# Kernel tuning notes

Hardware: AMD Instinct MI355X
Metric: run time of the kernel (lower is better)

The kernel has to match this reference:

```python
import jax, jax.numpy as jnp
import numpy as np
from jax import lax

B, FMAP, ENC, DEC, ATTN = 64, 512, 256, 512, 256
NUM_CLASSES, MAX_LEN = 96, 30
H, W = 8, 32


def setup_inputs() -> dict:
    key = jax.random.key(0)
    ks = jax.random.split(key, 20)
    s = 0.02
    inp = {
        "feature_map": jax.random.normal(ks[0], (B, FMAP, H, W), jnp.float32),
        "h0": jax.random.normal(ks[1], (2, B, DEC), jnp.float32),
        "c0": jax.random.normal(ks[2], (2, B, DEC), jnp.float32),
        "target": jax.random.randint(ks[3], (B, MAX_LEN), 0, NUM_CLASSES),
        "length": jax.random.randint(ks[4], (B,), 1, MAX_LEN),
        # embedding table: (num_classes+1, enc_dim)
        "emb": jax.random.normal(ks[5], (NUM_CLASSES + 1, ENC), jnp.float32) * s,
        # LSTM layer 0 (input ENC -> DEC), PyTorch gate order i,f,g,o
        "Wih0": jax.random.normal(ks[6], (4 * DEC, ENC), jnp.float32) * s,
        "Whh0": jax.random.normal(ks[7], (4 * DEC, DEC), jnp.float32) * s,
        "bih0": jnp.zeros((4 * DEC,), jnp.float32),
        "bhh0": jnp.zeros((4 * DEC,), jnp.float32),
        # LSTM layer 1 (DEC -> DEC)
        "Wih1": jax.random.normal(ks[8], (4 * DEC, DEC), jnp.float32) * s,
        "Whh1": jax.random.normal(ks[9], (4 * DEC, DEC), jnp.float32) * s,
        "bih1": jnp.zeros((4 * DEC,), jnp.float32),
        "bhh1": jnp.zeros((4 * DEC,), jnp.float32),
        # attention convs: 1x1 on hidden -> linear; 3x3 on fmap; 1x1 attn->1
        "e_lstm_w": jax.random.normal(ks[10], (ATTN, DEC), jnp.float32) * s,
        "e_lstm_b": jnp.zeros((ATTN,), jnp.float32),
        "e_fmap_w": jax.random.normal(ks[11], (ATTN, FMAP, 3, 3), jnp.float32) * s,
        "e_fmap_b": jnp.zeros((ATTN,), jnp.float32),
        "a_w": jax.random.normal(ks[12], (1, ATTN), jnp.float32) * s,
        "a_b": jnp.zeros((1,), jnp.float32),
        # fc: (dec+fmap) -> num_classes+2
        "fc_w": jax.random.normal(ks[13], (NUM_CLASSES + 2, DEC + FMAP), jnp.float32) * s,
        "fc_b": jnp.zeros((NUM_CLASSES + 2,), jnp.float32),
    }
    return inp


def _lstm_cell(x, h, c, Wih, Whh, bih, bhh):
    gates = x @ Wih.T + h @ Whh.T + (bih + bhh)
    i, f, g, o = jnp.split(gates, 4, axis=-1)
    i, f, o = jax.nn.sigmoid(i), jax.nn.sigmoid(f), jax.nn.sigmoid(o)
    c = f * c + i * jnp.tanh(g)
    h = o * jnp.tanh(c)
    return h, c


def reference(feature_map, h0, c0, target, length, emb,
              Wih0, Whh0, bih0, bhh0, Wih1, Whh1, bih1, bhh1,
              e_lstm_w, e_lstm_b, e_fmap_w, e_fmap_b, a_w, a_b, fc_w, fc_b):
    del length  # unused in forward math
    batch = feature_map.shape[0]
    # precompute 3x3 conv on the (constant) feature map once: [B, ATTN, H, W]
    e_fmap = lax.conv_general_dilated(
        feature_map, e_fmap_w, window_strides=(1, 1), padding="SAME",
        dimension_numbers=("NCHW", "OIHW", "NCHW")) + e_fmap_b[None, :, None, None]

    # teacher-forced input sequence: BOS token 0 then target -> [T+1, B]
    labels = jnp.concatenate(
        [jnp.zeros((batch, 1), target.dtype), target], axis=1).T  # [T+1, B]
    emb_seq = emb[labels]  # [T+1, B, ENC]

    def step(carry, x_t):
        h0_, c0_, h1_, c1_ = carry
        h0_, c0_ = _lstm_cell(x_t, h0_, c0_, Wih0, Whh0, bih0, bhh0)
        h1_, c1_ = _lstm_cell(h0_, h1_, c1_, Wih1, Whh1, bih1, bhh1)
        # additive conv attention
        e_h = h1_ @ e_lstm_w.T + e_lstm_b  # [B, ATTN]
        e = jnp.tanh(e_h[:, :, None, None] + e_fmap)  # [B, ATTN, H, W]
        score = jnp.einsum("bahw,a->bhw", e, a_w[0]) + a_b[0]  # [B, H, W]
        a = jax.nn.softmax(score.reshape(batch, -1), axis=-1)
        mask = a.reshape(batch, *score.shape[1:])  # [B, H, W]
        glimpse = jnp.einsum("bchw,bhw->bc", feature_map, mask)  # [B, FMAP]
        logit = jnp.concatenate([h1_, glimpse], axis=-1) @ fc_w.T + fc_b
        return (h0_, c0_, h1_, c1_), (logit, mask, glimpse)

    carry0 = (h0[0], c0[0], h0[1], c0[1])
    _, (logits, masks, glimpses) = lax.scan(step, carry0, emb_seq)
    # time-major -> batch-major
    logits = jnp.transpose(logits, (1, 0, 2))      # [B, T+1, C+2]
    masks = jnp.transpose(masks, (1, 0, 2, 3))     # [B, T+1, H, W]
    glimpses = jnp.transpose(glimpses, (1, 0, 2))  # [B, T+1, FMAP]
    return logits, masks, glimpses
```

## Files before the change

kernel.cpp:

```cpp
#include <hip/hip_runtime.h>
#include <hip/hip_bf16.h>


typedef __bf16 bf16_8 __attribute__((ext_vector_type(8)));
typedef __bf16 bf16_4 __attribute__((ext_vector_type(4)));
typedef float f32x4 __attribute__((ext_vector_type(4)));

typedef __hip_bfloat16 bf;

__device__ __forceinline__ float b2f(bf h) { return __bfloat162float(h); }
__device__ __forceinline__ bf f2b(float f) { return __float2bfloat16(f); }
__device__ __forceinline__ float sigm(float x) { return 1.0f / (1.0f + __expf(-x)); }
__device__ __forceinline__ float tanh_f(float x) { return 1.0f - 2.0f / (1.0f + __expf(2.0f * x)); }
__device__ __forceinline__ f32x4 mfma16(bf16_8 a, bf16_8 b, f32x4 c) {
    return __builtin_amdgcn_mfma_f32_16x16x32_bf16(a, b, c, 0, 0, 0);
}

__device__ __forceinline__ bf16_8 h_ld8(const bf* p) {
    typedef unsigned long long u64;
    union { u64 u[2]; bf16_8 v; } cv;
    cv.u[0] = __hip_atomic_load((const u64*)p, __ATOMIC_RELAXED, __HIP_MEMORY_SCOPE_AGENT);
    cv.u[1] = __hip_atomic_load((const u64*)p + 1, __ATOMIC_RELAXED, __HIP_MEMORY_SCOPE_AGENT);
    return cv.v;
}
__device__ __forceinline__ void h_st(bf* p, float f) {
    union { bf h; unsigned short u; } cv;
    cv.h = f2b(f);
    __hip_atomic_store((unsigned short*)p, cv.u, __ATOMIC_RELAXED, __HIP_MEMORY_SCOPE_AGENT);
}

#define NB 64
#define FMAP 512
#define ENC 256
#define DEC 512
#define ATTN 256
#define NC2 98
#define TT 31
#define HW 256
#define NROWS 1984
#define FSTRIDE 16


__global__ void k_detect(const int* __restrict__ t32, int* __restrict__ flags) {
    __shared__ int i64f;
    int tid = threadIdx.x;
    if (tid == 0) i64f = 1;
    __syncthreads();
    for (int i = tid; i < 960; i += 256)
        if (t32[2 * i + 1] != 0) i64f = 0;
    __syncthreads();
    if (tid == 0) { flags[0] = 0; flags[1] = i64f; }
}

#define N_CVT 17
struct CvtTab {
    const void* src[N_CVT];
    unsigned long long off[N_CVT];
    int n[N_CVT];
};

__global__ void k_cvt(CvtTab tab, unsigned char* __restrict__ ws) {
    int id = blockIdx.y;
    int n = tab.n[id];
    bf* dst = (bf*)(ws + tab.off[id]);
    const float* sf = (const float*)tab.src[id];
    for (int i = blockIdx.x * 256 + threadIdx.x; i < n; i += 256 * gridDim.x)
        dst[i] = f2b(sf[i]);
}


__global__ void k_init_state(const float* __restrict__ h0, const float* __restrict__ c0,
                             bf* __restrict__ h0_all, bf* __restrict__ h1_all,
                             float* __restrict__ c0f, float* __restrict__ c1f,
                             int* __restrict__ barf) {
    int i = blockIdx.x * 256 + threadIdx.x;
    if (i < 32768) barf[i] = 0;
    if (i >= NB * DEC) return;
    h0_all[i] = f2b(h0[i]);
    h1_all[i] = f2b(h0[NB * DEC + i]);
    c0f[i] = c0[i];
    c1f[i] = c0[NB * DEC + i];
}

__global__ void k_embed(const int* __restrict__ target, const bf* __restrict__ emb,
                        bf* __restrict__ x_seq, const int* __restrict__ flags) {
    int t = blockIdx.x, b = blockIdx.y, e = threadIdx.x;
    int lab = 0;
    if (t > 0) {
        int idx = b * 30 + (t - 1);
        lab = flags[1] ? target[2 * idx] : target[idx];
    }
    lab = min(max(lab, 0), 96);
    x_seq[(t * NB + b) * ENC + e] = emb[lab * ENC + e];
}

__global__ void k_wt(const bf* __restrict__ ew, bf* __restrict__ wt) {
    int dydx = blockIdx.x, a = blockIdx.y;
    for (int c = threadIdx.x; c < FMAP; c += 256)
        wt[(dydx * ATTN + a) * FMAP + c] = ew[(a * FMAP + c) * 9 + dydx];
}

__global__ __launch_bounds__(256) void k_padT(const float* __restrict__ fmapf,
                                              bf* __restrict__ fmapT) {
    __shared__ bf T3[64 * 258];
    int b = blockIdx.x, cq = blockIdx.y;
    int tid = threadIdx.x;
    for (int c_l = 0; c_l < 64; c_l++) {
        float v = fmapf[((size_t)(b * FMAP + cq * 64 + c_l)) * HW + tid];
        T3[c_l * 258 + tid] = f2b(v);
    }
    __syncthreads();
    int c_o = tid & 63, pg = tid >> 6;
    for (int it = 0; it < 64; it++) {
        int pos = it * 4 + pg;
        fmapT[((size_t)b * HW + pos) * FMAP + cq * 64 + c_o] = T3[c_o * 258 + pos];
    }
}

__global__ __launch_bounds__(256) void k_conv(const bf* __restrict__ fmapT,
                                              const bf* __restrict__ wt,
                                              const bf* __restrict__ efb,
                                              bf* __restrict__ ef) {
    __shared__ __align__(16) bf T[257 * 72];
    int b = blockIdx.x, aHalf = blockIdx.y, pHalf = blockIdx.z;
    int tid = threadIdx.x, wv = tid >> 6, lane = tid & 63;
    int q = lane >> 4, l = lane & 15;
    int abase = aHalf * 128 + wv * 32;

    for (int i = tid; i < 72; i += 256) T[256 * 72 + i] = f2b(0.0f);

    const bf* pb = fmapT + (size_t)b * HW * FMAP;
    f32x4 acc[2][8] = {};
    for (int cQ = 0; cQ < 8; cQ++) {
        __syncthreads();
#pragma unroll
        for (int j = 0; j < 8; j++) {
            int chunk = j * 256 + tid;
            int row = chunk >> 3, g = chunk & 7;
            *(bf16_8*)(T + row * 72 + g * 8) =
                *(const bf16_8*)(pb + (size_t)row * FMAP + cQ * 64 + g * 8);
        }
        __syncthreads();
        for (int dydx = 0; dydx < 9; dydx++) {
            int dy = dydx / 3, dx = dydx % 3;
            int rowv[8];
#pragma unroll
            for (int nt = 0; nt < 8; nt++) {
                int y = pHalf * 4 + (nt >> 1);
                int yp = y + dy - 1;
                int x = (nt & 1) * 16 + l;
                int xp = x + dx - 1;
                bool ok = (yp >= 0 && yp < 8 && xp >= 0 && xp < 32);
                rowv[nt] = ok ? (yp * 32 + xp) : 256;
            }
            const bf* wtd = wt + ((size_t)dydx * ATTN) * FMAP;
#pragma unroll
            for (int ck = 0; ck < 2; ck++) {
                int kg = cQ * 64 + ck * 32 + q * 8;
                bf16_8 afr[2];
#pragma unroll
                for (int mt = 0; mt < 2; mt++)
                    afr[mt] = *(const bf16_8*)(wtd + (abase + mt * 16 + l) * FMAP + kg);
#pragma unroll
                for (int nt = 0; nt < 8; nt++) {
                    bf16_8 bfr = *(const bf16_8*)(T + rowv[nt] * 72 + ck * 32 + q * 8);
                    acc[0][nt] = mfma16(afr[0], bfr, acc[0][nt]);
                    acc[1][nt] = mfma16(afr[1], bfr, acc[1][nt]);
                }
            }
        }
    }
#pragma unroll
    for (int mt = 0; mt < 2; mt++)
#pragma unroll
        for (int nt = 0; nt < 8; nt++) {
            int a0 = abase + mt * 16 + q * 4;
            int pos = pHalf * 128 + nt * 16 + l;
            bf16_4 o;
#pragma unroll
            for (int r = 0; r < 4; r++) o[r] = f2b(acc[mt][nt][r] + b2f(efb[a0 + r]));
            *(bf16_4*)(ef + ((size_t)(b * HW + pos)) * ATTN + a0) = o;
        }
}


struct SeqArgs {
    const bf *x_seq, *Wih0, *Whh0, *bih0, *bhh0, *Wih1, *Whh1, *bih1, *bhh1;
    bf *h0_all, *h1_all;
    float *c0f, *c1f;
    int *barf0, *barf1;
};

__device__ __forceinline__ void wait_flag(const int* p) {
    int guard = 0;
    while (__hip_atomic_load(p, __ATOMIC_RELAXED, __HIP_MEMORY_SCOPE_AGENT) == 0) {
        __builtin_amdgcn_s_sleep(1);
        if (++guard > (1 << 22)) break;
    }
}

__global__ __launch_bounds__(512) void k_seq(SeqArgs A) {
    __shared__ f32x4 red4[4][4][64];
    const int blk = blockIdx.x, tid = threadIdx.x;
    const int wave = tid >> 6, lane = tid & 63;
    const int q = lane >> 4, l = lane & 15;
    const int kh = wave >> 2, bt = wave & 3;
    const bool is0 = (blk >= 32);
    const int d0 = (is0 ? (blk - 32) : blk) * 16;
    const int d = d0 + l;

    float bi[4];
#pragma unroll
    for (int g = 0; g < 4; g++)
        bi[g] = is0 ? (b2f(A.bih0[g * 512 + d]) + b2f(A.bhh0[g * 512 + d]))
                    : (b2f(A.bih1[g * 512 + d]) + b2f(A.bhh1[g * 512 + d]));

    for (int s = 0; s <= 31; s++) {
        if (s >= 1) {
            if (is0) {
                if (s <= 30 && tid < 32)
                    wait_flag(A.barf0 + ((s - 1) * 32 + tid) * FSTRIDE);
            } else {
                if (tid < 32)
                    wait_flag(A.barf0 + ((s - 1) * 32 + tid) * FSTRIDE);
                else if (tid < 64 && s >= 2)
                    wait_flag(A.barf1 + ((s - 1) * 32 + (tid - 32)) * FSTRIDE);
            }
        }
        __syncthreads();

        if (is0) {
            if (s <= 30) {
                const bf* xt = A.x_seq + (size_t)s * NB * ENC;
                const bf* hprev = A.h0_all + (size_t)s * 32768;
                bf* hnew = A.h0_all + (size_t)(s + 1) * 32768;
                f32x4 acc[4] = {};
                if (kh == 0) {
                    bf16_8 af[8];
#pragma unroll
                    for (int i = 0; i < 8; i++)
                        af[i] = *(const bf16_8*)(xt + (bt * 16 + l) * ENC + i * 32 + q * 8);
#pragma unroll
                    for (int i = 0; i < 8; i++)
#pragma unroll
                        for (int g = 0; g < 4; g++)
                            acc[g] = mfma16(af[i],
                                *(const bf16_8*)(A.Wih0 + (g * 512 + d0 + l) * ENC + i * 32 + q * 8),
                                acc[g]);
                } else {
                    bf16_8 af[16];
#pragma unroll
                    for (int i = 0; i < 16; i++)
                        af[i] = h_ld8(hprev + (bt * 16 + l) * DEC + i * 32 + q * 8);
#pragma unroll
                    for (int i = 0; i < 16; i++)
#pragma unroll
                        for (int g = 0; g < 4; g++)
                            acc[g] = mfma16(af[i],
                                *(const bf16_8*)(A.Whh0 + (g * 512 + d0 + l) * DEC + i * 32 + q * 8),
                                acc[g]);
#pragma unroll
                    for (int g = 0; g < 4; g++) red4[bt][g][lane] = acc[g];
                }
                __syncthreads();
                if (kh == 0) {
#pragma unroll
                    for (int g = 0; g < 4; g++) acc[g] += red4[bt][g][lane];
#pragma unroll
                    for (int r = 0; r < 4; r++) {
                        int bb = bt * 16 + q * 4 + r;
                        float gi = sigm(acc[0][r] + bi[0]);
                        float gf = sigm(acc[1][r] + bi[1]);
                        float gg = tanh_f(acc[2][r] + bi[2]);
                        float go = sigm(acc[3][r] + bi[3]);
                        float c = gf * A.c0f[bb * DEC + d] + gi * gg;
                        A.c0f[bb * DEC + d] = c;
                        h_st(hnew + bb * DEC + d, go * tanh_f(c));
                    }
                }
            }
        } else {
            if (s >= 1) {
                const bf* h0n = A.h0_all + (size_t)s * 32768;
                const bf* h1p = A.h1_all + (size_t)(s - 1) * 32768;
                bf* h1n = A.h1_all + (size_t)s * 32768;
                const bf* Ain = kh ? h1p : h0n;
                const bf* Wp  = kh ? A.Whh1 : A.Wih1;
                f32x4 acc[4] = {};
                bf16_8 af[16];
#pragma unroll
                for (int i = 0; i < 16; i++)
                    af[i] = h_ld8(Ain + (bt * 16 + l) * DEC + i * 32 + q * 8);
#pragma unroll
                for (int i = 0; i < 16; i++)
#pragma unroll
                    for (int g = 0; g < 4; g++)
                        acc[g] = mfma16(af[i],
                            *(const bf16_8*)(Wp + (g * 512 + d0 + l) * DEC + i * 32 + q * 8),
                            acc[g]);
                if (kh == 1) {
#pragma unroll
                    for (int g = 0; g < 4; g++) red4[bt][g][lane] = acc[g];
                }
                __syncthreads();
                if (kh == 0) {
#pragma unroll
                    for (int g = 0; g < 4; g++) acc[g] += red4[bt][g][lane];
#pragma unroll
                    for (int r = 0; r < 4; r++) {
                        int bb = bt * 16 + q * 4 + r;
                        float gi = sigm(acc[0][r] + bi[0]);
                        float gf = sigm(acc[1][r] + bi[1]);
                        float gg = tanh_f(acc[2][r] + bi[2]);
                        float go = sigm(acc[3][r] + bi[3]);
                        float c = gf * A.c1f[bb * DEC + d] + gi * gg;
                        A.c1f[bb * DEC + d] = c;
                        h_st(h1n + bb * DEC + d, go * tanh_f(c));
                    }
                }
            }
        }

        __syncthreads();
        if (tid == 0) {
            if (is0) {
                if (s <= 30)
                    __hip_atomic_store(A.barf0 + (s * 32 + (blk - 32)) * FSTRIDE, 1,
                                       __ATOMIC_RELAXED, __HIP_MEMORY_SCOPE_AGENT);
            } else if (s >= 1) {
                __hip_atomic_store(A.barf1 + (s * 32 + blk) * FSTRIDE, 1,
                                   __ATOMIC_RELAXED, __HIP_MEMORY_SCOPE_AGENT);
            }
        }
    }
}


__global__ __launch_bounds__(256) void k_eh(const bf* __restrict__ h1_all,
                                            const bf* __restrict__ ew,
                                            const bf* __restrict__ eb,
                                            float* __restrict__ EHf) {
    int mtile = blockIdx.x, ntile = blockIdx.y;
    int tid = threadIdx.x, wv = tid >> 6, lane = tid & 63;
    int q = lane >> 4, l = lane & 15;
    const bf* A = h1_all + 32768;
    f32x4 acc[4] = {};
    for (int k0 = 0; k0 < DEC; k0 += 32) {
        bf16_8 af = *(const bf16_8*)(A + (size_t)(mtile * 64 + wv * 16 + l) * DEC + k0 + q * 8);
#pragma unroll
        for (int g = 0; g < 4; g++) {
            bf16_8 bfr = *(const bf16_8*)(ew + (size_t)(ntile * 64 + g * 16 + l) * DEC + k0 + q * 8);
            acc[g] = mfma16(af, bfr, acc[g]);
        }
    }
#pragma unroll
    for (int g = 0; g < 4; g++) {
        int col = ntile * 64 + g * 16 + l;
        float bias = b2f(eb[col]);
#pragma unroll
        for (int r = 0; r < 4; r++) {
            int m = mtile * 64 + wv * 16 + q * 4 + r;
            EHf[(size_t)m * ATTN + col] = acc[g][r] + bias;
        }
    }
}

__global__ __launch_bounds__(256) void k_score(const float* __restrict__ EHf,
                                               const bf* __restrict__ ef,
                                               const bf* __restrict__ a_w,
                                               float* __restrict__ out_masks,
                                               bf* __restrict__ maskb) {
    __shared__ float ehs[ATTN];
    __shared__ float aws[ATTN];
    __shared__ float red[256];
    int b = blockIdx.x, t = blockIdx.y, tid = threadIdx.x;

    ehs[tid] = EHf[(size_t)(t * NB + b) * ATTN + tid];
    aws[tid] = b2f(a_w[tid]);
    __syncthreads();

    const bf16_8* er = (const bf16_8*)(ef + ((size_t)b * HW + tid) * ATTN);
    float s0 = 0.f, s1 = 0.f, s2 = 0.f, s3 = 0.f;
#pragma unroll 4
    for (int a8 = 0; a8 < ATTN / 8; a8++) {
        bf16_8 e8 = er[a8];
        int a = a8 * 8;
        s0 += aws[a + 0] * tanh_f(ehs[a + 0] + (float)e8[0]);
        s1 += aws[a + 1] * tanh_f(ehs[a + 1] + (float)e8[1]);
        s2 += aws[a + 2] * tanh_f(ehs[a + 2] + (float)e8[2]);
        s3 += aws[a + 3] * tanh_f(ehs[a + 3] + (float)e8[3]);
        s0 += aws[a + 4] * tanh_f(ehs[a + 4] + (float)e8[4]);
        s1 += aws[a + 5] * tanh_f(ehs[a + 5] + (float)e8[5]);
        s2 += aws[a + 6] * tanh_f(ehs[a + 6] + (float)e8[6]);
        s3 += aws[a + 7] * tanh_f(ehs[a + 7] + (float)e8[7]);
    }
    float sc = (s0 + s1) + (s2 + s3);
    red[tid] = sc;
    __syncthreads();
    for (int off = 128; off > 0; off >>= 1) {
        if (tid < off) red[tid] = fmaxf(red[tid], red[tid + off]);
        __syncthreads();
    }
    float mx = red[0];
    __syncthreads();
    float ex = __expf(sc - mx);
    red[tid] = ex;
    __syncthreads();
    for (int off = 128; off > 0; off >>= 1) {
        if (tid < off) red[tid] += red[tid + off];
        __syncthreads();
    }
    float mk = ex / red[0];
    out_masks[((size_t)b * TT + t) * HW + tid] = mk;
    maskb[((size_t)b * 32 + t) * HW + tid] = f2b(mk);
}

__global__ __launch_bounds__(256) void k_glimpse(const float* __restrict__ fmapf,
                                                 const bf* __restrict__ maskb,
                                                 float* __restrict__ out_glimpses,
                                                 bf* __restrict__ glb) {
    int b = blockIdx.x, ctile = blockIdx.y;
    int tid = threadIdx.x, wv = tid >> 6, lane = tid & 63;
    int q = lane >> 4, l = lane & 15;
    const float* A = fmapf + (size_t)b * FMAP * HW + (size_t)(ctile * 64 + wv * 16 + l) * HW;
    const bf* B = maskb + (size_t)b * 32 * HW;
    f32x4 acc[2] = {};
    for (int k0 = 0; k0 < HW; k0 += 32) {
        const float* ap = A + k0 + q * 8;
        f32x4 v0 = *(const f32x4*)(ap);
        f32x4 v1 = *(const f32x4*)(ap + 4);
        bf16_8 af;
#pragma unroll
        for (int j = 0; j < 4; j++) { af[j] = (__bf16)v0[j]; af[4 + j] = (__bf16)v1[j]; }
#pragma unroll
        for (int tt = 0; tt < 2; tt++) {
            bf16_8 bfr = *(const bf16_8*)(B + (size_t)(tt * 16 + l) * HW + k0 + q * 8);
            acc[tt] = mfma16(af, bfr, acc[tt]);
        }
    }
#pragma unroll
    for (int tt = 0; tt < 2; tt++) {
        int t = tt * 16 + l;
        if (t > 30) continue;
#pragma unroll
        for (int r = 0; r < 4; r++) {
            int c = ctile * 64 + wv * 16 + q * 4 + r;
            float g = acc[tt][r];
            out_glimpses[((size_t)b * TT + t) * FMAP + c] = g;
            glb[(size_t)(t * NB + b) * FMAP + c] = f2b(g);
        }
    }
}

__global__ __launch_bounds__(256) void k_logits(const bf* __restrict__ h1_all,
                                                const bf* __restrict__ glb,
                                                const bf* __restrict__ fc_w,
                                                const bf* __restrict__ fc_b,
                                                float* __restrict__ out_logits) {
    int mtile = blockIdx.x, ntile = blockIdx.y;
    int tid = threadIdx.x, wv = tid >> 6, lane = tid & 63;
    int q = lane >> 4, l = lane & 15;
    const bf* A1 = h1_all + 32768;
    int cls = ntile * 16 + l;
    int clsc = min(cls, NC2 - 1);
    int rowA = mtile * 64 + wv * 16 + l;
    f32x4 acc = {};
    for (int k0 = 0; k0 < 1024; k0 += 32) {
        bf16_8 af;
        if (k0 < DEC)
            af = *(const bf16_8*)(A1 + (size_t)rowA * DEC + k0 + q * 8);
        else
            af = *(const bf16_8*)(glb + (size_t)rowA * FMAP + (k0 - DEC) + q * 8);
        bf16_8 bfr = *(const bf16_8*)(fc_w + (size_t)clsc * (DEC + FMAP) + k0 + q * 8);
        acc = mfma16(af, bfr, acc);
    }
    if (cls < NC2) {
        float bias = b2f(fc_b[cls]);
#pragma unroll
        for (int r = 0; r < 4; r++) {
            int m = mtile * 64 + wv * 16 + q * 4 + r;
            int bb = m & 63, t = m >> 6;
            out_logits[((size_t)bb * TT + t) * NC2 + cls] = acc[r] + bias;
        }
    }
}


extern "C" void kernel_launch(void* const* d_in, const int* in_sizes, int n_in,
                              void* d_out, int out_size, void* d_ws, size_t ws_size,
                              hipStream_t stream) {
    float* out = (float*)d_out;
    float* out_logits   = out;
    float* out_masks    = out + 64 * 31 * 98;
    float* out_glimpses = out + 64 * 31 * (98 + 256);

    unsigned char* ws = (unsigned char*)d_ws;
    unsigned long long off = 0;
    auto carve = [&](size_t bytes) {
        unsigned long long o = off;
        off = (off + bytes + 15ULL) & ~15ULL;
        return o;
    };

    unsigned long long o_flags = carve(64);
    unsigned long long o_bar = carve(131072);
    static const int cvt_in[N_CVT] = {5, 6, 7, 8, 9, 10, 11, 12, 13, 14, 15, 16, 17, 18, 19, 20, 21};
    static const int cvt_n[N_CVT] = {
        97 * 256, 2048 * 256, 2048 * 512, 2048, 2048,
        2048 * 512, 2048 * 512, 2048, 2048,
        256 * 512, 256, 256 * 512 * 9, 256, 256, 1,
        98 * 1024, 98
    };
    CvtTab tab;
    for (int i = 0; i < N_CVT; i++) {
        tab.src[i] = d_in[cvt_in[i]];
        tab.n[i] = cvt_n[i];
        tab.off[i] = carve((size_t)cvt_n[i] * 2);
    }
    const bf* emb_c    = (const bf*)(ws + tab.off[0]);
    const bf* Wih0_c   = (const bf*)(ws + tab.off[1]);
    const bf* Whh0_c   = (const bf*)(ws + tab.off[2]);
    const bf* bih0_c   = (const bf*)(ws + tab.off[3]);
    const bf* bhh0_c   = (const bf*)(ws + tab.off[4]);
    const bf* Wih1_c   = (const bf*)(ws + tab.off[5]);
    const bf* Whh1_c   = (const bf*)(ws + tab.off[6]);
    const bf* bih1_c   = (const bf*)(ws + tab.off[7]);
    const bf* bhh1_c   = (const bf*)(ws + tab.off[8]);
    const bf* e_lstm_w_c = (const bf*)(ws + tab.off[9]);
    const bf* e_lstm_b_c = (const bf*)(ws + tab.off[10]);
    const bf* e_fmap_w_c = (const bf*)(ws + tab.off[11]);
    const bf* e_fmap_b_c = (const bf*)(ws + tab.off[12]);
    const bf* a_w_c    = (const bf*)(ws + tab.off[13]);
    const bf* fc_w_c   = (const bf*)(ws + tab.off[15]);
    const bf* fc_b_c   = (const bf*)(ws + tab.off[16]);

    bf*    wt     = (bf*)(ws + carve((size_t)9 * 256 * 512 * 2));
    bf*    ef     = (bf*)(ws + carve((size_t)64 * 256 * 256 * 2));
    bf*    x_seq  = (bf*)(ws + carve((size_t)31 * 64 * 256 * 2));
    bf*    h0_all = (bf*)(ws + carve((size_t)33 * 65536));
    bf*    h1_all = (bf*)(ws + carve((size_t)32 * 65536));
    float* c0f    = (float*)(ws + carve(131072));
    float* c1f    = (float*)(ws + carve(131072));
    unsigned long long o_fmapT = carve((size_t)NB * HW * FMAP * 2);
    bf*    fmapT  = (bf*)(ws + o_fmapT);
    int*   flags  = (int*)(ws + o_flags);
    int*   barf0  = (int*)(ws + o_bar);
    int*   barf1  = (int*)(ws + o_bar + 65536);

    float* EHf    = (float*)(ws + o_fmapT);
    bf*    maskb  = (bf*)(ws + o_fmapT + 2031616ULL);
    bf*    glb    = (bf*)(ws + o_fmapT + 2031616ULL + 1048576ULL);

    k_detect<<<1, 256, 0, stream>>>((const int*)d_in[3], flags);
    k_cvt<<<dim3(256, N_CVT), 256, 0, stream>>>(tab, ws);
    k_init_state<<<128, 256, 0, stream>>>((const float*)d_in[1], (const float*)d_in[2],
                                          h0_all, h1_all, c0f, c1f, barf0);
    k_embed<<<dim3(TT, NB), 256, 0, stream>>>((const int*)d_in[3], emb_c, x_seq, flags);
    k_wt<<<dim3(9, ATTN), 256, 0, stream>>>(e_fmap_w_c, wt);
    k_padT<<<dim3(NB, 8), 256, 0, stream>>>((const float*)d_in[0], fmapT);
    k_conv<<<dim3(NB, 2, 2), 256, 0, stream>>>(fmapT, wt, e_fmap_b_c, ef);

    SeqArgs qa;
    qa.x_seq = x_seq; qa.Wih0 = Wih0_c; qa.Whh0 = Whh0_c;
    qa.bih0 = bih0_c; qa.bhh0 = bhh0_c;
    qa.Wih1 = Wih1_c; qa.Whh1 = Whh1_c; qa.bih1 = bih1_c; qa.bhh1 = bhh1_c;
    qa.h0_all = h0_all; qa.h1_all = h1_all; qa.c0f = c0f; qa.c1f = c1f;
    qa.barf0 = barf0; qa.barf1 = barf1;
    void* kargs[] = { (void*)&qa };
    hipLaunchCooperativeKernel((const void*)k_seq, dim3(64), dim3(512), kargs, 0, stream);

    k_eh<<<dim3(31, 4), 256, 0, stream>>>(h1_all, e_lstm_w_c, e_lstm_b_c, EHf);
    k_score<<<dim3(NB, TT), 256, 0, stream>>>(EHf, ef, a_w_c, out_masks, maskb);
    k_glimpse<<<dim3(NB, 8), 256, 0, stream>>>((const float*)d_in[0], maskb,
                                               out_glimpses, glb);
    k_logits<<<dim3(31, 7), 256, 0, stream>>>(h1_all, glb, fc_w_c, fc_b_c, out_logits);
}
```

Baseline: 1.104 ms.

## Repartition LSTM recurrence into batch-chunked blocks computing both layers per step

The cooperative LSTM kernel drops from 64 blocks (32 per layer, each covering all batch rows) to 32 blocks. Each block now owns a 16-row batch chunk and a 64-wide hidden slice, and computes layer-0 step s and layer-1 step s-1 together, reusing the loaded h0 fragments for both Whh0 and Wih1. Synchronisation collapses to a single flag array where each block waits on only 8 producers that share its batch chunk, instead of up to 64 flags across two arrays. This is meant to cut cross-block barrier latency and redundant h loads. The cost is fewer active CUs and more serial MFMA work per wave.

```diff
diff --git a/kernel.cpp b/kernel.cpp
--- a/kernel.cpp
+++ b/kernel.cpp
@@ -188,7 +188,7 @@
     const bf *x_seq, *Wih0, *Whh0, *bih0, *bhh0, *Wih1, *Whh1, *bih1, *bhh1;
     bf *h0_all, *h1_all;
     float *c0f, *c1f;
-    int *barf0, *barf1;
+    int *barf;
 };
 
 __device__ __forceinline__ void wait_flag(const int* p) {
@@ -200,138 +200,123 @@
 }
 
 __global__ __launch_bounds__(512) void k_seq(SeqArgs A) {
-    __shared__ f32x4 red4[4][4][64];
+    __shared__ float gl[2][16][16][16];
     const int blk = blockIdx.x, tid = threadIdx.x;
-    const int wave = tid >> 6, lane = tid & 63;
+    const int wv = tid >> 6, lane = tid & 63;
     const int q = lane >> 4, l = lane & 15;
-    const int kh = wave >> 2, bt = wave & 3;
-    const bool is0 = (blk >= 32);
-    const int d0 = (is0 ? (blk - 32) : blk) * 16;
-    const int d = d0 + l;
-
-    float bi[4];
-#pragma unroll
-    for (int g = 0; g < 4; g++)
-        bi[g] = is0 ? (b2f(A.bih0[g * 512 + d]) + b2f(A.bhh0[g * 512 + d]))
-                    : (b2f(A.bih1[g * 512 + d]) + b2f(A.bhh1[g * 512 + d]));
+    const int cc = blk & 3, jj = blk >> 2;
+    const int d0 = jj * 64;
+    const int nt0 = 2 * wv, nt1 = 2 * wv + 1;
+    const int wr0 = (nt0 >> 2) * 512 + d0 + (nt0 & 3) * 16 + l;
+    const int wr1 = (nt1 >> 2) * 512 + d0 + (nt1 & 3) * 16 + l;
+    const int dloc = tid & 63;
+    const int m0 = tid >> 6, m1 = 8 + (tid >> 6);
+    const int dglob = d0 + dloc;
 
     for (int s = 0; s <= 31; s++) {
+        if (s >= 1 && tid < 8)
+            wait_flag(A.barf + ((s - 1) * 32 + (cc + 4 * tid)) * FSTRIDE);
+        __syncthreads();
+
+        const bf* h0p = A.h0_all + (size_t)s * 32768 + cc * 16 * 512;
+        f32x4 a00 = {}, a01 = {}, a10 = {}, a11 = {};
+
+        if (s <= 30) {
+            const bf* xt = A.x_seq + ((size_t)s * 64 + cc * 16) * 256;
+#pragma unroll
+            for (int kk = 0; kk < 8; kk++) {
+                bf16_8 af = *(const bf16_8*)(xt + l * 256 + kk * 32 + q * 8);
+                a00 = mfma16(af, *(const bf16_8*)(A.Wih0 + (size_t)wr0 * 256 + kk * 32 + q * 8), a00);
+                a01 = mfma16(af, *(const bf16_8*)(A.Wih0 + (size_t)wr1 * 256 + kk * 32 + q * 8), a01);
+            }
+        }
+        {
+            bf16_8 af[16];
+#pragma unroll
+            for (int kk = 0; kk < 16; kk++)
+                af[kk] = h_ld8(h0p + l * 512 + kk * 32 + q * 8);
+            if (s <= 30) {
+#pragma unroll
+                for (int kk = 0; kk < 16; kk++) {
+                    a00 = mfma16(af[kk], *(const bf16_8*)(A.Whh0 + (size_t)wr0 * 512 + kk * 32 + q * 8), a00);
+                    a01 = mfma16(af[kk], *(const bf16_8*)(A.Whh0 + (size_t)wr1 * 512 + kk * 32 + q * 8), a01);
+                }
+            }
+            if (s >= 1) {
+#pragma unroll
+                for (int kk = 0; kk < 16; kk++) {
+                    a10 = mfma16(af[kk], *(const bf16_8*)(A.Wih1 + (size_t)wr0 * 512 + kk * 32 + q * 8), a10);
+                    a11 = mfma16(af[kk], *(const bf16_8*)(A.Wih1 + (size_t)wr1 * 512 + kk * 32 + q * 8), a11);
+                }
+            }
+        }
         if (s >= 1) {
-            if (is0) {
-                if (s <= 30 && tid < 32)
-                    wait_flag(A.barf0 + ((s - 1) * 32 + tid) * FSTRIDE);
-            } else {
-                if (tid < 32)
-                    wait_flag(A.barf0 + ((s - 1) * 32 + tid) * FSTRIDE);
-                else if (tid < 64 && s >= 2)
-                    wait_flag(A.barf1 + ((s - 1) * 32 + (tid - 32)) * FSTRIDE);
-            }
-        }
-        __syncthreads();
-
-        if (is0) {
-            if (s <= 30) {
-                const bf* xt = A.x_seq + (size_t)s * NB * ENC;
-                const bf* hprev = A.h0_all + (size_t)s * 32768;
-                bf* hnew = A.h0_all + (size_t)(s + 1) * 32768;
-                f32x4 acc[4] = {};
-                if (kh == 0) {
-                    bf16_8 af[8];
-#pragma unroll
-                    for (int i = 0; i < 8; i++)
-                        af[i] = *(const bf16_8*)(xt + (bt * 16 + l) * ENC + i * 32 + q * 8);
-#pragma unroll
-                    for (int i = 0; i < 8; i++)
-#pragma unroll
-                        for (int g = 0; g < 4; g++)
-                            acc[g] = mfma16(af[i],
-                                *(const bf16_8*)(A.Wih0 + (g * 512 + d0 + l) * ENC + i * 32 + q * 8),
-                                acc[g]);
-                } else {
-                    bf16_8 af[16];
-#pragma unroll
-                    for (int i = 0; i < 16; i++)
-                        af[i] = h_ld8(hprev + (bt * 16 + l) * DEC + i * 32 + q * 8);
-#pragma unroll
-                    for (int i = 0; i < 16; i++)
-#pragma unroll
-                        for (int g = 0; g < 4; g++)
-                            acc[g] = mfma16(af[i],
-                                *(const bf16_8*)(A.Whh0 + (g * 512 + d0 + l) * DEC + i * 32 + q * 8),
-                                acc[g]);
-#pragma unroll
-                    for (int g = 0; g < 4; g++) red4[bt][g][lane] = acc[g];
+            const bf* h1p = A.h1_all + (size_t)(s - 1) * 32768 + cc * 16 * 512;
+#pragma unroll
+            for (int kk = 0; kk < 16; kk++) {
+                bf16_8 af = h_ld8(h1p + l * 512 + kk * 32 + q * 8);
+                a10 = mfma16(af, *(const bf16_8*)(A.Whh1 + (size_t)wr0 * 512 + kk * 32 + q * 8), a10);
+                a11 = mfma16(af, *(const bf16_8*)(A.Whh1 + (size_t)wr1 * 512 + kk * 32 + q * 8), a11);
+            }
+        }
+        if (s <= 30) {
+#pragma unroll
+            for (int r = 0; r < 4; r++) {
+                gl[0][nt0][q * 4 + r][l] = a00[r];
+                gl[0][nt1][q * 4 + r][l] = a01[r];
+            }
+        }
+        if (s >= 1) {
+#pragma unroll
+            for (int r = 0; r < 4; r++) {
+                gl[1][nt0][q * 4 + r][l] = a10[r];
+                gl[1][nt1][q * 4 + r][l] = a11[r];
+            }
+        }
+        __syncthreads();
+
+        if (s <= 30) {
+            bf* hnew = A.h0_all + (size_t)(s + 1) * 32768 + cc * 16 * 512;
+#pragma unroll
+            for (int half = 0; half < 2; half++) {
+                int m = half ? m1 : m0;
+                float gate[4];
+#pragma unroll
+                for (int g = 0; g < 4; g++) {
+                    float bi = b2f(A.bih0[g * 512 + dglob]) + b2f(A.bhh0[g * 512 + dglob]);
+                    gate[g] = gl[0][g * 4 + (dloc >> 4)][m][dloc & 15] + bi;
                 }
-                __syncthreads();
-                if (kh == 0) {
-#pragma unroll
-                    for (int g = 0; g < 4; g++) acc[g] += red4[bt][g][lane];
-#pragma unroll
-                    for (int r = 0; r < 4; r++) {
-                        int bb = bt * 16 + q * 4 + r;
-                        float gi = sigm(acc[0][r] + bi[0]);
-                        float gf = sigm(acc[1][r] + bi[1]);
-                        float gg = tanh_f(acc[2][r] + bi[2]);
-                        float go = sigm(acc[3][r] + bi[3]);
-                        float c = gf * A.c0f[bb * DEC + d] + gi * gg;
-                        A.c0f[bb * DEC + d] = c;
-                        h_st(hnew + bb * DEC + d, go * tanh_f(c));
-                    }
+                float gi = sigm(gate[0]), gf = sigm(gate[1]);
+                float gg = tanh_f(gate[2]), go = sigm(gate[3]);
+                size_t ci = (size_t)(cc * 16 + m) * 512 + dglob;
+                float c = gf * A.c0f[ci] + gi * gg;
+                A.c0f[ci] = c;
+                h_st(hnew + (m * 512 + dglob), go * tanh_f(c));
+            }
+        }
+        if (s >= 1) {
+            bf* h1n = A.h1_all + (size_t)s * 32768 + cc * 16 * 512;
+#pragma unroll
+            for (int half = 0; half < 2; half++) {
+                int m = half ? m1 : m0;
+                float gate[4];
+#pragma unroll
+                for (int g = 0; g < 4; g++) {
+                    float bi = b2f(A.bih1[g * 512 + dglob]) + b2f(A.bhh1[g * 512 + dglob]);
+                    gate[g] = gl[1][g * 4 + (dloc >> 4)][m][dloc & 15] + bi;
                 }
-            }
-        } else {
-            if (s >= 1) {
-                const bf* h0n = A.h0_all + (size_t)s * 32768;
-                const bf* h1p = A.h1_all + (size_t)(s - 1) * 32768;
-                bf* h1n = A.h1_all + (size_t)s * 32768;
-                const bf* Ain = kh ? h1p : h0n;
-                const bf* Wp  = kh ? A.Whh1 : A.Wih1;
-                f32x4 acc[4] = {};
-                bf16_8 af[16];
-#pragma unroll
-                for (int i = 0; i < 16; i++)
-                    af[i] = h_ld8(Ain + (bt * 16 + l) * DEC + i * 32 + q * 8);
-#pragma unroll
-                for (int i = 0; i < 16; i++)
-#pragma unroll
-                    for (int g = 0; g < 4; g++)
-                        acc[g] = mfma16(af[i],
-                            *(const bf16_8*)(Wp + (g * 512 + d0 + l) * DEC + i * 32 + q * 8),
-                            acc[g]);
-                if (kh == 1) {
-#pragma unroll
-                    for (int g = 0; g < 4; g++) red4[bt][g][lane] = acc[g];
-                }
-                __syncthreads();
-                if (kh == 0) {
-#pragma unroll
-                    for (int g = 0; g < 4; g++) acc[g] += red4[bt][g][lane];
-#pragma unroll
-                    for (int r = 0; r < 4; r++) {
-                        int bb = bt * 16 + q * 4 + r;
-                        float gi = sigm(acc[0][r] + bi[0]);
-                        float gf = sigm(acc[1][r] + bi[1]);
-                        float gg = tanh_f(acc[2][r] + bi[2]);
-                        float go = sigm(acc[3][r] + bi[3]);
-                        float c = gf * A.c1f[bb * DEC + d] + gi * gg;
-                        A.c1f[bb * DEC + d] = c;
-                        h_st(h1n + bb * DEC + d, go * tanh_f(c));
-                    }
-                }
-            }
-        }
-
-        __syncthreads();
-        if (tid == 0) {
-            if (is0) {
-                if (s <= 30)
-                    __hip_atomic_store(A.barf0 + (s * 32 + (blk - 32)) * FSTRIDE, 1,
-                                       __ATOMIC_RELAXED, __HIP_MEMORY_SCOPE_AGENT);
-            } else if (s >= 1) {
-                __hip_atomic_store(A.barf1 + (s * 32 + blk) * FSTRIDE, 1,
-                                   __ATOMIC_RELAXED, __HIP_MEMORY_SCOPE_AGENT);
-            }
-        }
+                float gi = sigm(gate[0]), gf = sigm(gate[1]);
+                float gg = tanh_f(gate[2]), go = sigm(gate[3]);
+                size_t ci = (size_t)(cc * 16 + m) * 512 + dglob;
+                float c = gf * A.c1f[ci] + gi * gg;
+                A.c1f[ci] = c;
+                h_st(h1n + (m * 512 + dglob), go * tanh_f(c));
+            }
+        }
+        __syncthreads();
+        if (tid == 0)
+            __hip_atomic_store(A.barf + (s * 32 + blk) * FSTRIDE, 1,
+                               __ATOMIC_RELAXED, __HIP_MEMORY_SCOPE_AGENT);
     }
 }
 
@@ -544,8 +529,7 @@
     unsigned long long o_fmapT = carve((size_t)NB * HW * FMAP * 2);
     bf*    fmapT  = (bf*)(ws + o_fmapT);
     int*   flags  = (int*)(ws + o_flags);
-    int*   barf0  = (int*)(ws + o_bar);
-    int*   barf1  = (int*)(ws + o_bar + 65536);
+    int*   barf   = (int*)(ws + o_bar);
 
     float* EHf    = (float*)(ws + o_fmapT);
     bf*    maskb  = (bf*)(ws + o_fmapT + 2031616ULL);
@@ -554,7 +538,7 @@
     k_detect<<<1, 256, 0, stream>>>((const int*)d_in[3], flags);
     k_cvt<<<dim3(256, N_CVT), 256, 0, stream>>>(tab, ws);
     k_init_state<<<128, 256, 0, stream>>>((const float*)d_in[1], (const float*)d_in[2],
-                                          h0_all, h1_all, c0f, c1f, barf0);
+                                          h0_all, h1_all, c0f, c1f, barf);
     k_embed<<<dim3(TT, NB), 256, 0, stream>>>((const int*)d_in[3], emb_c, x_seq, flags);
     k_wt<<<dim3(9, ATTN), 256, 0, stream>>>(e_fmap_w_c, wt);
     k_padT<<<dim3(NB, 8), 256, 0, stream>>>((const float*)d_in[0], fmapT);
@@ -565,9 +549,9 @@
     qa.bih0 = bih0_c; qa.bhh0 = bhh0_c;
     qa.Wih1 = Wih1_c; qa.Whh1 = Whh1_c; qa.bih1 = bih1_c; qa.bhh1 = bhh1_c;
     qa.h0_all = h0_all; qa.h1_all = h1_all; qa.c0f = c0f; qa.c1f = c1f;
-    qa.barf0 = barf0; qa.barf1 = barf1;
+    qa.barf = barf;
     void* kargs[] = { (void*)&qa };
-    hipLaunchCooperativeKernel((const void*)k_seq, dim3(64), dim3(512), kargs, 0, stream);
+    hipLaunchCooperativeKernel((const void*)k_seq, dim3(32), dim3(512), kargs, 0, stream);
 
     k_eh<<<dim3(31, 4), 256, 0, stream>>>(h1_all, e_lstm_w_c, e_lstm_b_c, EHf);
     k_score<<<dim3(NB, TT), 256, 0, stream>>>(EHf, ef, a_w_c, out_masks, maskb);
```

After: 1.749 ms. 1.58x slower.
